# Performance work log

Hardware: AMD Instinct MI355X
Metric: run time of the kernel (lower is better)

Reference implementation:

```python
import jax, jax.numpy as jnp
import numpy as np

B, S, D, H, DFF = 2, 2048, 1024, 16, 4096
HD = D // H
EPS = 1e-5


def setup_inputs() -> dict:
    key = jax.random.key(0)
    ks = jax.random.split(key, 8)
    s = lambda fan_in: 1.0 / np.sqrt(fan_in)
    return {
        "x": jax.random.normal(ks[0], (B, S, D), jnp.float32),
        "ln1_g": jnp.ones((D,), jnp.float32),
        "ln1_b": jnp.zeros((D,), jnp.float32),
        "Wq": jax.random.normal(ks[1], (D, D), jnp.float32) * s(D),
        "Wk": jax.random.normal(ks[2], (D, D), jnp.float32) * s(D),
        "Wv": jax.random.normal(ks[3], (D, D), jnp.float32) * s(D),
        "Wo": jax.random.normal(ks[4], (D, D), jnp.float32) * s(D),
        "bo": jnp.zeros((D,), jnp.float32),
        "ln2_g": jnp.ones((D,), jnp.float32),
        "ln2_b": jnp.zeros((D,), jnp.float32),
        "W1": jax.random.normal(ks[5], (D, DFF), jnp.float32) * s(D),
        "b1": jnp.zeros((DFF,), jnp.float32),
        "W2": jax.random.normal(ks[6], (DFF, D), jnp.float32) * s(DFF),
        "b2": jnp.zeros((D,), jnp.float32),
    }


def _layernorm(x, g, b):
    mu = jnp.mean(x, axis=-1, keepdims=True)
    var = jnp.var(x, axis=-1, keepdims=True)
    return (x - mu) * jax.lax.rsqrt(var + EPS) * g + b


def reference(x, ln1_g, ln1_b, Wq, Wk, Wv, Wo, bo, ln2_g, ln2_b, W1, b1, W2, b2):
    # --- pre-LN + causal multi-head attention + residual ---
    h = _layernorm(x, ln1_g, ln1_b)
    q = (h @ Wq).reshape(B, S, H, HD).transpose(0, 2, 1, 3)  # [B,H,S,hd]
    k = (h @ Wk).reshape(B, S, H, HD).transpose(0, 2, 1, 3)
    v = (h @ Wv).reshape(B, S, H, HD).transpose(0, 2, 1, 3)
    scores = jnp.einsum("bhqd,bhkd->bhqk", q, k) / jnp.sqrt(jnp.float32(HD))
    causal = jnp.triu(jnp.ones((S, S), bool), k=1)  # True above diagonal -> masked
    scores = jnp.where(causal, -jnp.inf, scores)
    attn = jax.nn.softmax(scores, axis=-1)  # dropout is identity at inference
    ctx = jnp.einsum("bhqk,bhkd->bhqd", attn, v)
    ctx = ctx.transpose(0, 2, 1, 3).reshape(B, S, D)
    x = x + ctx @ Wo + bo
    # --- pre-LN + MLP + residual ---
    h = _layernorm(x, ln2_g, ln2_b)
    h = jax.nn.gelu(h @ W1 + b1, approximate=False)  # torch nn.GELU default = exact
    x = x + h @ W2 + b2
    return x
```

## Files before the change

### kernel.cpp

```cpp
#include <hip/hip_runtime.h>
#include <hip/hip_bf16.h>
#include <math.h>

using bf16 = __hip_bfloat16;
typedef short bf16x8 __attribute__((ext_vector_type(8)));
typedef float f32x4 __attribute__((ext_vector_type(4)));

static constexpr int B = 2, S = 2048, D = 1024, H = 16, HD = 64, DFF = 4096;
static constexpr int NR = B * S;
static constexpr int DQ = 3072;
static constexpr float EPS = 1e-5f;

__device__ __forceinline__ bf16 f2b(float v) { return __float2bfloat16(v); }

typedef __attribute__((address_space(1))) const void* gp1_t;
typedef __attribute__((address_space(3))) void* sp3_t;
__device__ __forceinline__ void gld_lds16(const bf16* g, bf16* l) {
    __builtin_amdgcn_global_load_lds((gp1_t)(const void*)g, (sp3_t)(void*)l, 16, 0, 0);
}

__global__ __launch_bounds__(256) void convT_kernel(const float* __restrict__ src,
                                                    bf16* __restrict__ dst,
                                                    int K, int N) {
    __shared__ float tile[64][65];
    const int k0 = blockIdx.x * 64, n0 = blockIdx.y * 64;
    const int tid = threadIdx.x;
    const int r = tid >> 4, c = (tid & 15) * 4;
#pragma unroll
    for (int rr = 0; rr < 64; rr += 16) {
        float4 v = *(const float4*)&src[(size_t)(k0 + r + rr) * N + n0 + c];
        tile[r + rr][c] = v.x; tile[r + rr][c + 1] = v.y;
        tile[r + rr][c + 2] = v.z; tile[r + rr][c + 3] = v.w;
    }
    __syncthreads();
    const int n = tid >> 2, ks = (tid & 3) * 16;
    union { bf16 h[16]; int4 v2[2]; } o;
#pragma unroll
    for (int i = 0; i < 16; ++i) o.h[i] = f2b(tile[ks + i][n]);
    bf16* dp = &dst[(size_t)(n0 + n) * K + k0 + ks];
    *(int4*)dp = o.v2[0];
    *(int4*)(dp + 8) = o.v2[1];
}

__global__ __launch_bounds__(256) void ln_kernel(const float* __restrict__ x,
                                                 const float* __restrict__ g,
                                                 const float* __restrict__ b,
                                                 bf16* __restrict__ out) {
    const int row = blockIdx.x;
    const int tid = threadIdx.x;
    const float4 v4 = ((const float4*)(x + (size_t)row * D))[tid];
    float v[4] = {v4.x, v4.y, v4.z, v4.w};
    float s = v[0] + v[1] + v[2] + v[3];
    float sq = v[0] * v[0] + v[1] * v[1] + v[2] * v[2] + v[3] * v[3];
#pragma unroll
    for (int off = 32; off >= 1; off >>= 1) {
        s += __shfl_xor(s, off);
        sq += __shfl_xor(sq, off);
    }
    __shared__ float ssum[4], ssq[4];
    const int wave = tid >> 6;
    if ((tid & 63) == 0) { ssum[wave] = s; ssq[wave] = sq; }
    __syncthreads();
    s = ssum[0] + ssum[1] + ssum[2] + ssum[3];
    sq = ssq[0] + ssq[1] + ssq[2] + ssq[3];
    const float mu = s * (1.0f / D);
    const float var = sq * (1.0f / D) - mu * mu;
    const float rstd = rsqrtf(var + EPS);
    bf16* orow = out + (size_t)row * D;
#pragma unroll
    for (int i = 0; i < 4; ++i) {
        const int c = tid * 4 + i;
        orow[c] = f2b((v[i] - mu) * rstd * g[c] + b[c]);
    }
}

template <int EPI, int BN, int TPB>
__global__ __launch_bounds__(256) void gemm_bt(const bf16* __restrict__ A,
                                               const bf16* __restrict__ Bt,
                                               const float* __restrict__ bias,
                                               const float* __restrict__ res,
                                               void* __restrict__ Cv,
                                               int M, int N, int K) {
    constexpr int NTW = BN / 32;
    constexpr int ASZ = 128 * 32, BSZ = BN * 32;
    constexpr int CST = BN + 8;
    constexpr int BUFE = 2 * (ASZ + BSZ);
    constexpr int STGE = (EPI == 1) ? 0 : 128 * CST;
    constexpr int SMEM = BUFE > STGE ? BUFE : STGE;
    __shared__ __align__(16) bf16 smem[SMEM];

    const int Mtiles = M / 128;
    const int p = blockIdx.x;
    const int tm = p % Mtiles;
    const int tn0 = (p / Mtiles) * TPB;
    const int tid = threadIdx.x;
    const int wave = tid >> 6, lane = tid & 63;
    const int wm = wave >> 1, wn = wave & 1;
    const int quad = lane >> 4, l16 = lane & 15;

    const int s_row = tid >> 2, s_seg = (tid & 3) * 8;
    const size_t K64 = (size_t)64 * K;
    const int nk = K / 32;

    for (int tp = 0; tp < TPB; ++tp) {
        const int tn = tn0 + tp;
        if (tp) __syncthreads();

        f32x4 acc[4][NTW];
#pragma unroll
        for (int i = 0; i < 4; ++i)
#pragma unroll
            for (int j = 0; j < NTW; ++j) acc[i][j] = (f32x4){0.f, 0.f, 0.f, 0.f};

        const bf16* Ap = A + (size_t)(tm * 128 + s_row) * K + s_seg;
        const bf16* Bp = Bt + (size_t)(tn * BN + s_row) * K + s_seg;

        gld_lds16(Ap, smem + tid * 8);
        gld_lds16(Ap + K64, smem + (256 + tid) * 8);
        gld_lds16(Bp, smem + 2 * ASZ + tid * 8);
        if constexpr (BN == 128) gld_lds16(Bp + K64, smem + 2 * ASZ + (256 + tid) * 8);
        Ap += 32;
        Bp += 32;

        for (int kt = 0; kt < nk; ++kt) {
            const int cur = kt & 1, nxt = cur ^ 1;
            bf16* Acur = smem + cur * ASZ;
            bf16* Bcur = smem + 2 * ASZ + cur * BSZ;
            __syncthreads();
            if (kt + 1 < nk) {
                bf16* Anxt = smem + nxt * ASZ;
                bf16* Bnxt = smem + 2 * ASZ + nxt * BSZ;
                gld_lds16(Ap, Anxt + tid * 8);
                gld_lds16(Ap + K64, Anxt + (256 + tid) * 8);
                gld_lds16(Bp, Bnxt + tid * 8);
                if constexpr (BN == 128) gld_lds16(Bp + K64, Bnxt + (256 + tid) * 8);
                Ap += 32;
                Bp += 32;
            }

            bf16x8 aF[4], bF[NTW];
#pragma unroll
            for (int mt = 0; mt < 4; ++mt)
                aF[mt] = *(const bf16x8*)(Acur + (wm * 64 + mt * 16 + l16) * 32 + quad * 8);
#pragma unroll
            for (int nt = 0; nt < NTW; ++nt)
                bF[nt] = *(const bf16x8*)(Bcur + (wn * (BN / 2) + nt * 16 + l16) * 32 + quad * 8);
#pragma unroll
            for (int mt = 0; mt < 4; ++mt)
#pragma unroll
                for (int nt = 0; nt < NTW; ++nt)
                    acc[mt][nt] = __builtin_amdgcn_mfma_f32_16x16x32_bf16(
                        aF[mt], bF[nt], acc[mt][nt], 0, 0, 0);
        }

        if constexpr (EPI == 1) {
#pragma unroll
            for (int nt = 0; nt < NTW; ++nt) {
                const int col = tn * BN + wn * (BN / 2) + nt * 16 + l16;
                const float bv = bias[col];
#pragma unroll
                for (int mt = 0; mt < 4; ++mt) {
                    const int row0 = tm * 128 + wm * 64 + mt * 16 + quad * 4;
#pragma unroll
                    for (int j = 0; j < 4; ++j) {
                        const size_t idx = (size_t)(row0 + j) * N + col;
                        ((float*)Cv)[idx] = acc[mt][nt][j] + bv + res[idx];
                    }
                }
            }
        } else {
            __syncthreads();
#pragma unroll
            for (int nt = 0; nt < NTW; ++nt) {
                const int ccol = wn * (BN / 2) + nt * 16 + l16;
                float bv = 0.f;
                if (EPI == 2) bv = bias[tn * BN + ccol];
#pragma unroll
                for (int mt = 0; mt < 4; ++mt) {
                    const int r0 = wm * 64 + mt * 16 + quad * 4;
#pragma unroll
                    for (int j = 0; j < 4; ++j) {
                        float v = acc[mt][nt][j];
                        if (EPI == 2) {
                            v += bv;
                            v = 0.5f * v * (1.0f + erff(v * 0.70710678118654752f));
                        }
                        smem[(r0 + j) * CST + ccol] = f2b(v);
                    }
                }
            }
            __syncthreads();
            constexpr int NI4 = BN / 16;
            bf16* crow = (bf16*)Cv + (size_t)(tm * 128) * N + tn * BN;
#pragma unroll
            for (int i = 0; i < NI4; ++i) {
                const int gid = i * 256 + tid;
                const int row = gid / (BN / 8), c8 = gid % (BN / 8);
                const int4 val = *(const int4*)(smem + row * CST + c8 * 8);
                *(int4*)(crow + (size_t)row * N + c8 * 8) = val;
            }
        }
    }
}

__global__ __launch_bounds__(512) void fattn_kernel(const bf16* __restrict__ QKV,
                                                    bf16* __restrict__ ctx) {
    const int id = blockIdx.x;
    const int pair = id >> 5;
    const int bh = id & 31;
    const int b = bh >> 4, h = bh & (H - 1);
    const int tid = threadIdx.x;
    const int wave = tid >> 6, lane = tid & 63;
    const int quad = lane >> 4, l16 = lane & 15;
    const bf16* Qp = QKV + (size_t)b * S * DQ + h * HD;
    const bf16* Kp = Qp + D;
    const bf16* Vp = Qp + 2 * D;

    __shared__ __align__(16) bf16 Ks[2][64 * 64];
    __shared__ __align__(16) bf16 Vt[2][64][72];
    __shared__ __align__(16) bf16 Ps[128][76];

    const int keyA = tid >> 3, dsA = ((tid & 7) ^ (keyA & 7)) * 8;

    const int tiles[2] = {S / 128 - 1 - pair, pair};
#pragma unroll
    for (int ti = 0; ti < 2; ++ti) {
        const int t = tiles[ti];
        const int q0 = t * 128;
        const bf16* qg = Qp + (size_t)(q0 + wave * 16 + l16) * DQ + quad * 8;
        const bf16x8 aQ0 = *(const bf16x8*)(qg);
        const bf16x8 aQ1 = *(const bf16x8*)(qg + 32);

        f32x4 O[4];
#pragma unroll
        for (int nt = 0; nt < 4; ++nt) O[nt] = (f32x4){0.f, 0.f, 0.f, 0.f};
        float m[4] = {-3.0e38f, -3.0e38f, -3.0e38f, -3.0e38f};
        float l[4] = {0.f, 0.f, 0.f, 0.f};

        __syncthreads();
        gld_lds16(Kp + (size_t)keyA * DQ + dsA, Ks[0] + tid * 8);
        {
            const bf16* vg = Vp + (size_t)lane * DQ + wave * 8;
            union { int4 v; bf16 hh[8]; } u;
            u.v = *(const int4*)vg;
#pragma unroll
            for (int i = 0; i < 8; ++i) Vt[0][wave * 8 + i][lane] = u.hh[i];
        }

        const int nch = 2 * t + 2;
        for (int c = 0; c < nch; ++c) {
            const int cur = c & 1, nxt = cur ^ 1;
            __syncthreads();
            union { int4 v; bf16 hh[8]; } u;
            if (c < nch - 1) {
                const int k1 = (c + 1) * 64;
                gld_lds16(Kp + (size_t)(k1 + keyA) * DQ + dsA, Ks[nxt] + tid * 8);
                u.v = *(const int4*)(Vp + (size_t)(k1 + lane) * DQ + wave * 8);
            }

            f32x4 sc[4];
#pragma unroll
            for (int nt = 0; nt < 4; ++nt) {
                const int r = nt * 16 + l16;
                const bf16x8 bK0 = *(const bf16x8*)(Ks[cur] + (r * 8 + (quad ^ (r & 7))) * 8);
                const bf16x8 bK1 = *(const bf16x8*)(Ks[cur] + (r * 8 + ((4 + quad) ^ (r & 7))) * 8);
                f32x4 z = (f32x4){0.f, 0.f, 0.f, 0.f};
                z = __builtin_amdgcn_mfma_f32_16x16x32_bf16(aQ0, bK0, z, 0, 0, 0);
                z = __builtin_amdgcn_mfma_f32_16x16x32_bf16(aQ1, bK1, z, 0, 0, 0);
                sc[nt] = z;
            }
#pragma unroll
            for (int nt = 0; nt < 4; ++nt)
#pragma unroll
                for (int j = 0; j < 4; ++j) sc[nt][j] *= 0.125f;
            if (c >= 2 * t) {
                const int kbase = (c - 2 * t) * 64;
#pragma unroll
                for (int nt = 0; nt < 4; ++nt) {
                    const int rel_k = kbase + nt * 16 + l16;
#pragma unroll
                    for (int j = 0; j < 4; ++j)
                        if (rel_k > wave * 16 + quad * 4 + j) sc[nt][j] = -3.0e38f;
                }
            }
            float al[4];
#pragma unroll
            for (int j = 0; j < 4; ++j) {
                float mx = fmaxf(fmaxf(sc[0][j], sc[1][j]), fmaxf(sc[2][j], sc[3][j]));
#pragma unroll
                for (int off = 1; off <= 8; off <<= 1) mx = fmaxf(mx, __shfl_xor(mx, off));
                const float mn = fmaxf(m[j], mx);
                al[j] = __expf(m[j] - mn);
                m[j] = mn;
                float rs = 0.f;
#pragma unroll
                for (int nt = 0; nt < 4; ++nt) {
                    sc[nt][j] = __expf(sc[nt][j] - mn);
                    rs += sc[nt][j];
                }
#pragma unroll
                for (int off = 1; off <= 8; off <<= 1) rs += __shfl_xor(rs, off);
                l[j] = l[j] * al[j] + rs;
            }
#pragma unroll
            for (int nt = 0; nt < 4; ++nt)
#pragma unroll
                for (int j = 0; j < 4; ++j)
                    Ps[wave * 16 + quad * 4 + j][nt * 16 + l16] = f2b(sc[nt][j]);
            asm volatile("s_waitcnt lgkmcnt(0)" ::: "memory");
            const bf16x8 aP0 = *(const bf16x8*)&Ps[wave * 16 + l16][quad * 8];
            const bf16x8 aP1 = *(const bf16x8*)&Ps[wave * 16 + l16][32 + quad * 8];
#pragma unroll
            for (int nt = 0; nt < 4; ++nt)
#pragma unroll
                for (int j = 0; j < 4; ++j) O[nt][j] *= al[j];
#pragma unroll
            for (int nt = 0; nt < 4; ++nt) {
                const bf16x8 bV0 = *(const bf16x8*)&Vt[cur][nt * 16 + l16][quad * 8];
                const bf16x8 bV1 = *(const bf16x8*)&Vt[cur][nt * 16 + l16][32 + quad * 8];
                O[nt] = __builtin_amdgcn_mfma_f32_16x16x32_bf16(aP0, bV0, O[nt], 0, 0, 0);
                O[nt] = __builtin_amdgcn_mfma_f32_16x16x32_bf16(aP1, bV1, O[nt], 0, 0, 0);
            }
            if (c < nch - 1) {
#pragma unroll
                for (int i = 0; i < 8; ++i) Vt[nxt][wave * 8 + i][lane] = u.hh[i];
            }
        }

        const size_t hoC = (size_t)b * S * D + h * HD;
        float rl[4];
#pragma unroll
        for (int j = 0; j < 4; ++j) rl[j] = 1.0f / l[j];
#pragma unroll
        for (int nt = 0; nt < 4; ++nt)
#pragma unroll
            for (int j = 0; j < 4; ++j)
                ctx[hoC + (size_t)(q0 + wave * 16 + quad * 4 + j) * D + nt * 16 + l16] =
                    f2b(O[nt][j] * rl[j]);
    }
}

extern "C" void kernel_launch(void* const* d_in, const int* in_sizes, int n_in,
                              void* d_out, int out_size, void* d_ws, size_t ws_size,
                              hipStream_t stream) {
    const float* x     = (const float*)d_in[0];
    const float* ln1_g = (const float*)d_in[1];
    const float* ln1_b = (const float*)d_in[2];
    const float* Wq    = (const float*)d_in[3];
    const float* Wk    = (const float*)d_in[4];
    const float* Wv    = (const float*)d_in[5];
    const float* Wo    = (const float*)d_in[6];
    const float* bo    = (const float*)d_in[7];
    const float* ln2_g = (const float*)d_in[8];
    const float* ln2_b = (const float*)d_in[9];
    const float* W1    = (const float*)d_in[10];
    const float* b1    = (const float*)d_in[11];
    const float* W2    = (const float*)d_in[12];
    const float* b2    = (const float*)d_in[13];
    float* out = (float*)d_out;

    char* ws = (char*)d_ws;
    const size_t MB = (size_t)1 << 20;
    bf16* h     = (bf16*)(ws + 0 * MB);
    bf16* W1T   = (bf16*)(ws + 0 * MB);
    bf16* QKVb  = (bf16*)(ws + 8 * MB);
    bf16* hff   = (bf16*)(ws + 8 * MB);
    bf16* ctx   = (bf16*)(ws + 32 * MB);
    bf16* h2    = (bf16*)(ws + 40 * MB);
    bf16* WqkvT = (bf16*)(ws + 48 * MB);
    bf16* WoT   = (bf16*)(ws + 54 * MB);
    bf16* W2T   = (bf16*)(ws + 56 * MB);

    dim3 gt(16, 16);
    convT_kernel<<<gt, 256, 0, stream>>>(Wq, WqkvT,                 D, D);
    convT_kernel<<<gt, 256, 0, stream>>>(Wk, WqkvT + (size_t)D * D, D, D);
    convT_kernel<<<gt, 256, 0, stream>>>(Wv, WqkvT + (size_t)2 * D * D, D, D);
    convT_kernel<<<gt, 256, 0, stream>>>(Wo, WoT, D, D);
    convT_kernel<<<dim3(64, 16), 256, 0, stream>>>(W2, W2T, DFF, D);
    ln_kernel<<<NR, 256, 0, stream>>>(x, ln1_g, ln1_b, h);
    gemm_bt<0, 128, 1><<<(NR / 128) * (DQ / 128), 256, 0, stream>>>(
        h, WqkvT, nullptr, nullptr, QKVb, NR, DQ, D);
    convT_kernel<<<dim3(16, 64), 256, 0, stream>>>(W1, W1T, D, DFF);
    fattn_kernel<<<dim3((S / 128 / 2) * B * H), 512, 0, stream>>>(QKVb, ctx);
    gemm_bt<1, 64, 1><<<(NR / 128) * (D / 64), 256, 0, stream>>>(
        ctx, WoT, bo, x, out, NR, D, D);
    ln_kernel<<<NR, 256, 0, stream>>>(out, ln2_g, ln2_b, h2);
    gemm_bt<2, 128, 2><<<(NR / 128) * (DFF / 128) / 2, 256, 0, stream>>>(
        h2, W1T, b1, nullptr, hff, NR, DFF, D);
    gemm_bt<1, 64, 1><<<(NR / 128) * (D / 64), 256, 0, stream>>>(
        hff, W2T, b2, out, out, NR, D, DFF);
}
```

Baseline: 389.0 us.

## Add 256x128 GEMM kernel for QKV/FFN1 and split attention tiles per block

Introduces a 512-thread gemm256 kernel with 256x128 output tiles for the QKV projection and the W1+GELU GEMM. The larger tiles raise operand reuse per LDS load, and the bf16 epilogue is staged through LDS in two halves. The attention kernel now processes one query tile per block instead of a paired long/short tile, launching twice as many blocks ordered longest-first for load balance. The old bf16-output path is removed from gemm_bt, which now keeps only the fp32 residual epilogue. Trade-offs are fewer GEMM blocks with heavier register use, and attention blocks of uneven length.

```diff
diff --git a/kernel.cpp b/kernel.cpp
--- a/kernel.cpp
+++ b/kernel.cpp
@@ -74,6 +74,109 @@
     }
 }
 
+template <int EPI>
+__global__ __launch_bounds__(512) void gemm256(const bf16* __restrict__ A,
+                                               const bf16* __restrict__ Bt,
+                                               const float* __restrict__ bias,
+                                               bf16* __restrict__ C,
+                                               int M, int N, int K) {
+    constexpr int ASZ = 256 * 32, BSZ = 128 * 32;
+    constexpr int CST = 128 + 8;
+    __shared__ __align__(16) bf16 smem[2 * (ASZ + BSZ)];
+
+    const int Mtiles = M / 256;
+    const int p = blockIdx.x;
+    const int tm = p % Mtiles;
+    const int tn = p / Mtiles;
+    const int tid = threadIdx.x;
+    const int wave = tid >> 6, lane = tid & 63;
+    const int wm = wave >> 1, wn = wave & 1;
+    const int quad = lane >> 4, l16 = lane & 15;
+
+    f32x4 acc[4][4];
+#pragma unroll
+    for (int i = 0; i < 4; ++i)
+#pragma unroll
+        for (int j = 0; j < 4; ++j) acc[i][j] = (f32x4){0.f, 0.f, 0.f, 0.f};
+
+    const int s_row = tid >> 2, s_seg = (tid & 3) * 8;
+    const bf16* ApLo = A + (size_t)(tm * 256 + s_row) * K + s_seg;
+    const size_t K128 = (size_t)128 * K;
+    const bf16* Bp = Bt + (size_t)(tn * 128 + s_row) * K + s_seg;
+
+    gld_lds16(ApLo, smem + tid * 8);
+    gld_lds16(ApLo + K128, smem + (512 + tid) * 8);
+    gld_lds16(Bp, smem + 2 * ASZ + tid * 8);
+    ApLo += 32;
+    Bp += 32;
+
+    const int nk = K / 32;
+    for (int kt = 0; kt < nk; ++kt) {
+        const int cur = kt & 1, nxt = cur ^ 1;
+        bf16* Acur = smem + cur * ASZ;
+        bf16* Bcur = smem + 2 * ASZ + cur * BSZ;
+        __syncthreads();
+        if (kt + 1 < nk) {
+            bf16* Anxt = smem + nxt * ASZ;
+            bf16* Bnxt = smem + 2 * ASZ + nxt * BSZ;
+            gld_lds16(ApLo, Anxt + tid * 8);
+            gld_lds16(ApLo + K128, Anxt + (512 + tid) * 8);
+            gld_lds16(Bp, Bnxt + tid * 8);
+            ApLo += 32;
+            Bp += 32;
+        }
+
+        bf16x8 aF[4], bF[4];
+#pragma unroll
+        for (int mt = 0; mt < 4; ++mt)
+            aF[mt] = *(const bf16x8*)(Acur + (wm * 64 + mt * 16 + l16) * 32 + quad * 8);
+#pragma unroll
+        for (int nt = 0; nt < 4; ++nt)
+            bF[nt] = *(const bf16x8*)(Bcur + (wn * 64 + nt * 16 + l16) * 32 + quad * 8);
+#pragma unroll
+        for (int mt = 0; mt < 4; ++mt)
+#pragma unroll
+            for (int nt = 0; nt < 4; ++nt)
+                acc[mt][nt] = __builtin_amdgcn_mfma_f32_16x16x32_bf16(
+                    aF[mt], bF[nt], acc[mt][nt], 0, 0, 0);
+    }
+
+#pragma unroll
+    for (int hh = 0; hh < 2; ++hh) {
+        __syncthreads();
+        if ((wm >> 1) == hh) {
+#pragma unroll
+            for (int nt = 0; nt < 4; ++nt) {
+                const int ccol = wn * 64 + nt * 16 + l16;
+                float bv = 0.f;
+                if (EPI == 2) bv = bias[tn * 128 + ccol];
+#pragma unroll
+                for (int mt = 0; mt < 4; ++mt) {
+                    const int r0 = (wm & 1) * 64 + mt * 16 + quad * 4;
+#pragma unroll
+                    for (int j = 0; j < 4; ++j) {
+                        float v = acc[mt][nt][j];
+                        if (EPI == 2) {
+                            v += bv;
+                            v = 0.5f * v * (1.0f + erff(v * 0.70710678118654752f));
+                        }
+                        smem[(r0 + j) * CST + ccol] = f2b(v);
+                    }
+                }
+            }
+        }
+        __syncthreads();
+        bf16* crow = C + (size_t)(tm * 256 + hh * 128) * N + tn * 128;
+#pragma unroll
+        for (int i = 0; i < 4; ++i) {
+            const int gid = i * 512 + tid;
+            const int row = gid >> 4, c8 = gid & 15;
+            const int4 val = *(const int4*)(smem + row * CST + c8 * 8);
+            *(int4*)(crow + (size_t)row * N + c8 * 8) = val;
+        }
+    }
+}
+
 template <int EPI, int BN, int TPB>
 __global__ __launch_bounds__(256) void gemm_bt(const bf16* __restrict__ A,
                                                const bf16* __restrict__ Bt,
@@ -83,11 +186,7 @@
                                                int M, int N, int K) {
     constexpr int NTW = BN / 32;
     constexpr int ASZ = 128 * 32, BSZ = BN * 32;
-    constexpr int CST = BN + 8;
-    constexpr int BUFE = 2 * (ASZ + BSZ);
-    constexpr int STGE = (EPI == 1) ? 0 : 128 * CST;
-    constexpr int SMEM = BUFE > STGE ? BUFE : STGE;
-    __shared__ __align__(16) bf16 smem[SMEM];
+    __shared__ __align__(16) bf16 smem[2 * (ASZ + BSZ)];
 
     const int Mtiles = M / 128;
     const int p = blockIdx.x;
@@ -153,51 +252,18 @@
                         aF[mt], bF[nt], acc[mt][nt], 0, 0, 0);
         }
 
-        if constexpr (EPI == 1) {
-#pragma unroll
-            for (int nt = 0; nt < NTW; ++nt) {
-                const int col = tn * BN + wn * (BN / 2) + nt * 16 + l16;
-                const float bv = bias[col];
-#pragma unroll
-                for (int mt = 0; mt < 4; ++mt) {
-                    const int row0 = tm * 128 + wm * 64 + mt * 16 + quad * 4;
-#pragma unroll
-                    for (int j = 0; j < 4; ++j) {
-                        const size_t idx = (size_t)(row0 + j) * N + col;
-                        ((float*)Cv)[idx] = acc[mt][nt][j] + bv + res[idx];
-                    }
+#pragma unroll
+        for (int nt = 0; nt < NTW; ++nt) {
+            const int col = tn * BN + wn * (BN / 2) + nt * 16 + l16;
+            const float bv = bias[col];
+#pragma unroll
+            for (int mt = 0; mt < 4; ++mt) {
+                const int row0 = tm * 128 + wm * 64 + mt * 16 + quad * 4;
+#pragma unroll
+                for (int j = 0; j < 4; ++j) {
+                    const size_t idx = (size_t)(row0 + j) * N + col;
+                    ((float*)Cv)[idx] = acc[mt][nt][j] + bv + res[idx];
                 }
-            }
-        } else {
-            __syncthreads();
-#pragma unroll
-            for (int nt = 0; nt < NTW; ++nt) {
-                const int ccol = wn * (BN / 2) + nt * 16 + l16;
-                float bv = 0.f;
-                if (EPI == 2) bv = bias[tn * BN + ccol];
-#pragma unroll
-                for (int mt = 0; mt < 4; ++mt) {
-                    const int r0 = wm * 64 + mt * 16 + quad * 4;
-#pragma unroll
-                    for (int j = 0; j < 4; ++j) {
-                        float v = acc[mt][nt][j];
-                        if (EPI == 2) {
-                            v += bv;
-                            v = 0.5f * v * (1.0f + erff(v * 0.70710678118654752f));
-                        }
-                        smem[(r0 + j) * CST + ccol] = f2b(v);
-                    }
-                }
-            }
-            __syncthreads();
-            constexpr int NI4 = BN / 16;
-            bf16* crow = (bf16*)Cv + (size_t)(tm * 128) * N + tn * BN;
-#pragma unroll
-            for (int i = 0; i < NI4; ++i) {
-                const int gid = i * 256 + tid;
-                const int row = gid / (BN / 8), c8 = gid % (BN / 8);
-                const int4 val = *(const int4*)(smem + row * CST + c8 * 8);
-                *(int4*)(crow + (size_t)row * N + c8 * 8) = val;
             }
         }
     }
@@ -206,8 +272,9 @@
 __global__ __launch_bounds__(512) void fattn_kernel(const bf16* __restrict__ QKV,
                                                     bf16* __restrict__ ctx) {
     const int id = blockIdx.x;
-    const int pair = id >> 5;
     const int bh = id & 31;
+    const int k = id >> 5;
+    const int t = (k < 8) ? 15 - k : k - 8;
     const int b = bh >> 4, h = bh & (H - 1);
     const int tid = threadIdx.x;
     const int wave = tid >> 6, lane = tid & 63;
@@ -222,122 +289,116 @@
 
     const int keyA = tid >> 3, dsA = ((tid & 7) ^ (keyA & 7)) * 8;
 
-    const int tiles[2] = {S / 128 - 1 - pair, pair};
-#pragma unroll
-    for (int ti = 0; ti < 2; ++ti) {
-        const int t = tiles[ti];
-        const int q0 = t * 128;
-        const bf16* qg = Qp + (size_t)(q0 + wave * 16 + l16) * DQ + quad * 8;
-        const bf16x8 aQ0 = *(const bf16x8*)(qg);
-        const bf16x8 aQ1 = *(const bf16x8*)(qg + 32);
-
-        f32x4 O[4];
-#pragma unroll
-        for (int nt = 0; nt < 4; ++nt) O[nt] = (f32x4){0.f, 0.f, 0.f, 0.f};
-        float m[4] = {-3.0e38f, -3.0e38f, -3.0e38f, -3.0e38f};
-        float l[4] = {0.f, 0.f, 0.f, 0.f};
-
+    const int q0 = t * 128;
+    const bf16* qg = Qp + (size_t)(q0 + wave * 16 + l16) * DQ + quad * 8;
+    const bf16x8 aQ0 = *(const bf16x8*)(qg);
+    const bf16x8 aQ1 = *(const bf16x8*)(qg + 32);
+
+    f32x4 O[4];
+#pragma unroll
+    for (int nt = 0; nt < 4; ++nt) O[nt] = (f32x4){0.f, 0.f, 0.f, 0.f};
+    float m[4] = {-3.0e38f, -3.0e38f, -3.0e38f, -3.0e38f};
+    float l[4] = {0.f, 0.f, 0.f, 0.f};
+
+    gld_lds16(Kp + (size_t)keyA * DQ + dsA, Ks[0] + tid * 8);
+    {
+        const bf16* vg = Vp + (size_t)lane * DQ + wave * 8;
+        union { int4 v; bf16 hh[8]; } u;
+        u.v = *(const int4*)vg;
+#pragma unroll
+        for (int i = 0; i < 8; ++i) Vt[0][wave * 8 + i][lane] = u.hh[i];
+    }
+
+    const int nch = 2 * t + 2;
+    for (int c = 0; c < nch; ++c) {
+        const int cur = c & 1, nxt = cur ^ 1;
         __syncthreads();
-        gld_lds16(Kp + (size_t)keyA * DQ + dsA, Ks[0] + tid * 8);
-        {
-            const bf16* vg = Vp + (size_t)lane * DQ + wave * 8;
-            union { int4 v; bf16 hh[8]; } u;
-            u.v = *(const int4*)vg;
-#pragma unroll
-            for (int i = 0; i < 8; ++i) Vt[0][wave * 8 + i][lane] = u.hh[i];
-        }
-
-        const int nch = 2 * t + 2;
-        for (int c = 0; c < nch; ++c) {
-            const int cur = c & 1, nxt = cur ^ 1;
-            __syncthreads();
-            union { int4 v; bf16 hh[8]; } u;
-            if (c < nch - 1) {
-                const int k1 = (c + 1) * 64;
-                gld_lds16(Kp + (size_t)(k1 + keyA) * DQ + dsA, Ks[nxt] + tid * 8);
-                u.v = *(const int4*)(Vp + (size_t)(k1 + lane) * DQ + wave * 8);
+        union { int4 v; bf16 hh[8]; } u;
+        if (c < nch - 1) {
+            const int k1 = (c + 1) * 64;
+            gld_lds16(Kp + (size_t)(k1 + keyA) * DQ + dsA, Ks[nxt] + tid * 8);
+            u.v = *(const int4*)(Vp + (size_t)(k1 + lane) * DQ + wave * 8);
+        }
+
+        f32x4 sc[4];
+#pragma unroll
+        for (int nt = 0; nt < 4; ++nt) {
+            const int r = nt * 16 + l16;
+            const bf16x8 bK0 = *(const bf16x8*)(Ks[cur] + (r * 8 + (quad ^ (r & 7))) * 8);
+            const bf16x8 bK1 = *(const bf16x8*)(Ks[cur] + (r * 8 + ((4 + quad) ^ (r & 7))) * 8);
+            f32x4 z = (f32x4){0.f, 0.f, 0.f, 0.f};
+            z = __builtin_amdgcn_mfma_f32_16x16x32_bf16(aQ0, bK0, z, 0, 0, 0);
+            z = __builtin_amdgcn_mfma_f32_16x16x32_bf16(aQ1, bK1, z, 0, 0, 0);
+            sc[nt] = z;
+        }
+#pragma unroll
+        for (int nt = 0; nt < 4; ++nt)
+#pragma unroll
+            for (int j = 0; j < 4; ++j) sc[nt][j] *= 0.125f;
+        if (c >= 2 * t) {
+            const int kbase = (c - 2 * t) * 64;
+#pragma unroll
+            for (int nt = 0; nt < 4; ++nt) {
+                const int rel_k = kbase + nt * 16 + l16;
+#pragma unroll
+                for (int j = 0; j < 4; ++j)
+                    if (rel_k > wave * 16 + quad * 4 + j) sc[nt][j] = -3.0e38f;
             }
-
-            f32x4 sc[4];
+        }
+        float al[4];
+#pragma unroll
+        for (int j = 0; j < 4; ++j) {
+            float mx = fmaxf(fmaxf(sc[0][j], sc[1][j]), fmaxf(sc[2][j], sc[3][j]));
+#pragma unroll
+            for (int off = 1; off <= 8; off <<= 1) mx = fmaxf(mx, __shfl_xor(mx, off));
+            const float mn = fmaxf(m[j], mx);
+            al[j] = __expf(m[j] - mn);
+            m[j] = mn;
+            float rs = 0.f;
 #pragma unroll
             for (int nt = 0; nt < 4; ++nt) {
-                const int r = nt * 16 + l16;
-                const bf16x8 bK0 = *(const bf16x8*)(Ks[cur] + (r * 8 + (quad ^ (r & 7))) * 8);
-                const bf16x8 bK1 = *(const bf16x8*)(Ks[cur] + (r * 8 + ((4 + quad) ^ (r & 7))) * 8);
-                f32x4 z = (f32x4){0.f, 0.f, 0.f, 0.f};
-                z = __builtin_amdgcn_mfma_f32_16x16x32_bf16(aQ0, bK0, z, 0, 0, 0);
-                z = __builtin_amdgcn_mfma_f32_16x16x32_bf16(aQ1, bK1, z, 0, 0, 0);
-                sc[nt] = z;
+                sc[nt][j] = __expf(sc[nt][j] - mn);
+                rs += sc[nt][j];
             }
 #pragma unroll
-            for (int nt = 0; nt < 4; ++nt)
-#pragma unroll
-                for (int j = 0; j < 4; ++j) sc[nt][j] *= 0.125f;
-            if (c >= 2 * t) {
-                const int kbase = (c - 2 * t) * 64;
-#pragma unroll
-                for (int nt = 0; nt < 4; ++nt) {
-                    const int rel_k = kbase + nt * 16 + l16;
-#pragma unroll
-                    for (int j = 0; j < 4; ++j)
-                        if (rel_k > wave * 16 + quad * 4 + j) sc[nt][j] = -3.0e38f;
-                }
-            }
-            float al[4];
-#pragma unroll
-            for (int j = 0; j < 4; ++j) {
-                float mx = fmaxf(fmaxf(sc[0][j], sc[1][j]), fmaxf(sc[2][j], sc[3][j]));
-#pragma unroll
-                for (int off = 1; off <= 8; off <<= 1) mx = fmaxf(mx, __shfl_xor(mx, off));
-                const float mn = fmaxf(m[j], mx);
-                al[j] = __expf(m[j] - mn);
-                m[j] = mn;
-                float rs = 0.f;
-#pragma unroll
-                for (int nt = 0; nt < 4; ++nt) {
-                    sc[nt][j] = __expf(sc[nt][j] - mn);
-                    rs += sc[nt][j];
-                }
-#pragma unroll
-                for (int off = 1; off <= 8; off <<= 1) rs += __shfl_xor(rs, off);
-                l[j] = l[j] * al[j] + rs;
-            }
-#pragma unroll
-            for (int nt = 0; nt < 4; ++nt)
-#pragma unroll
-                for (int j = 0; j < 4; ++j)
-                    Ps[wave * 16 + quad * 4 + j][nt * 16 + l16] = f2b(sc[nt][j]);
-            asm volatile("s_waitcnt lgkmcnt(0)" ::: "memory");
-            const bf16x8 aP0 = *(const bf16x8*)&Ps[wave * 16 + l16][quad * 8];
-            const bf16x8 aP1 = *(const bf16x8*)&Ps[wave * 16 + l16][32 + quad * 8];
-#pragma unroll
-            for (int nt = 0; nt < 4; ++nt)
-#pragma unroll
-                for (int j = 0; j < 4; ++j) O[nt][j] *= al[j];
-#pragma unroll
-            for (int nt = 0; nt < 4; ++nt) {
-                const bf16x8 bV0 = *(const bf16x8*)&Vt[cur][nt * 16 + l16][quad * 8];
-                const bf16x8 bV1 = *(const bf16x8*)&Vt[cur][nt * 16 + l16][32 + quad * 8];
-                O[nt] = __builtin_amdgcn_mfma_f32_16x16x32_bf16(aP0, bV0, O[nt], 0, 0, 0);
-                O[nt] = __builtin_amdgcn_mfma_f32_16x16x32_bf16(aP1, bV1, O[nt], 0, 0, 0);
-            }
-            if (c < nch - 1) {
-#pragma unroll
-                for (int i = 0; i < 8; ++i) Vt[nxt][wave * 8 + i][lane] = u.hh[i];
-            }
-        }
-
-        const size_t hoC = (size_t)b * S * D + h * HD;
-        float rl[4];
-#pragma unroll
-        for (int j = 0; j < 4; ++j) rl[j] = 1.0f / l[j];
+            for (int off = 1; off <= 8; off <<= 1) rs += __shfl_xor(rs, off);
+            l[j] = l[j] * al[j] + rs;
+        }
 #pragma unroll
         for (int nt = 0; nt < 4; ++nt)
 #pragma unroll
             for (int j = 0; j < 4; ++j)
-                ctx[hoC + (size_t)(q0 + wave * 16 + quad * 4 + j) * D + nt * 16 + l16] =
-                    f2b(O[nt][j] * rl[j]);
-    }
+                Ps[wave * 16 + quad * 4 + j][nt * 16 + l16] = f2b(sc[nt][j]);
+        asm volatile("s_waitcnt lgkmcnt(0)" ::: "memory");
+        const bf16x8 aP0 = *(const bf16x8*)&Ps[wave * 16 + l16][quad * 8];
+        const bf16x8 aP1 = *(const bf16x8*)&Ps[wave * 16 + l16][32 + quad * 8];
+#pragma unroll
+        for (int nt = 0; nt < 4; ++nt)
+#pragma unroll
+            for (int j = 0; j < 4; ++j) O[nt][j] *= al[j];
+#pragma unroll
+        for (int nt = 0; nt < 4; ++nt) {
+            const bf16x8 bV0 = *(const bf16x8*)&Vt[cur][nt * 16 + l16][quad * 8];
+            const bf16x8 bV1 = *(const bf16x8*)&Vt[cur][nt * 16 + l16][32 + quad * 8];
+            O[nt] = __builtin_amdgcn_mfma_f32_16x16x32_bf16(aP0, bV0, O[nt], 0, 0, 0);
+            O[nt] = __builtin_amdgcn_mfma_f32_16x16x32_bf16(aP1, bV1, O[nt], 0, 0, 0);
+        }
+        if (c < nch - 1) {
+#pragma unroll
+            for (int i = 0; i < 8; ++i) Vt[nxt][wave * 8 + i][lane] = u.hh[i];
+        }
+    }
+
+    const size_t hoC = (size_t)b * S * D + h * HD;
+    float rl[4];
+#pragma unroll
+    for (int j = 0; j < 4; ++j) rl[j] = 1.0f / l[j];
+#pragma unroll
+    for (int nt = 0; nt < 4; ++nt)
+#pragma unroll
+        for (int j = 0; j < 4; ++j)
+            ctx[hoC + (size_t)(q0 + wave * 16 + quad * 4 + j) * D + nt * 16 + l16] =
+                f2b(O[nt][j] * rl[j]);
 }
 
 extern "C" void kernel_launch(void* const* d_in, const int* in_sizes, int n_in,
@@ -378,15 +439,15 @@
     convT_kernel<<<gt, 256, 0, stream>>>(Wo, WoT, D, D);
     convT_kernel<<<dim3(64, 16), 256, 0, stream>>>(W2, W2T, DFF, D);
     ln_kernel<<<NR, 256, 0, stream>>>(x, ln1_g, ln1_b, h);
-    gemm_bt<0, 128, 1><<<(NR / 128) * (DQ / 128), 256, 0, stream>>>(
-        h, WqkvT, nullptr, nullptr, QKVb, NR, DQ, D);
+    gemm256<0><<<(NR / 256) * (DQ / 128), 512, 0, stream>>>(
+        h, WqkvT, nullptr, QKVb, NR, DQ, D);
     convT_kernel<<<dim3(16, 64), 256, 0, stream>>>(W1, W1T, D, DFF);
-    fattn_kernel<<<dim3((S / 128 / 2) * B * H), 512, 0, stream>>>(QKVb, ctx);
+    fattn_kernel<<<dim3((S / 128) * B * H), 512, 0, stream>>>(QKVb, ctx);
     gemm_bt<1, 64, 1><<<(NR / 128) * (D / 64), 256, 0, stream>>>(
         ctx, WoT, bo, x, out, NR, D, D);
     ln_kernel<<<NR, 256, 0, stream>>>(out, ln2_g, ln2_b, h2);
-    gemm_bt<2, 128, 2><<<(NR / 128) * (DFF / 128) / 2, 256, 0, stream>>>(
-        h2, W1T, b1, nullptr, hff, NR, DFF, D);
+    gemm256<2><<<(NR / 256) * (DFF / 128), 512, 0, stream>>>(
+        h2, W1T, b1, hff, NR, DFF, D);
     gemm_bt<1, 64, 1><<<(NR / 128) * (D / 64), 256, 0, stream>>>(
         hff, W2T, b2, out, out, NR, D, DFF);
 }
```

After: 382.1 us. Within noise of the previous version (-1.8%).
